# Kernel optimization log

Hardware: AMD Instinct MI355X
Metric: run time of the kernel (lower is better)

## Reference

```python
import jax, jax.numpy as jnp
import numpy as np

IN_DIM = 784   # 28*28
N_FEAT = 100
MW = 20
MP = 100
S = 30
N = 2048
BETA = 0.9
THRESH = 1.0


def setup_inputs() -> dict:
    key = jax.random.key(0)
    ks = jax.random.split(key, 6)
    X = jax.random.uniform(ks[0], (N, IN_DIM), jnp.float32)
    r1 = (1.0 / IN_DIM) ** 0.5
    W1 = jax.random.uniform(ks[1], (IN_DIM, N_FEAT), jnp.float32, -r1, r1)
    B1 = jax.random.uniform(ks[2], (N_FEAT,), jnp.float32, -r1, r1)
    r2 = (1.0 / N_FEAT) ** 0.5
    # all mw windows concatenated: (n_feat, mw*mp)
    W2 = jax.random.uniform(ks[3], (N_FEAT, MW * MP), jnp.float32, -r2, r2)
    B2 = jax.random.uniform(ks[4], (MW * MP,), jnp.float32, -r2, r2)
    # uniform noise for Bernoulli rate coding (spikegen.rate)
    U = jax.random.uniform(ks[5], (S, N, N_FEAT), jnp.float32)
    return {"X": X, "W1": W1, "B1": B1, "W2": W2, "B2": B2, "U": U}


def reference(X, W1, B1, W2, B2, U):
    # Feature layer: linear -> sigmoid(./3) -> Bernoulli rate-coded spikes
    Z_prob = jax.nn.sigmoid((X @ W1 + B1) / 3.0)          # (N, F)
    Z_spk = (U < Z_prob[None]).astype(X.dtype)             # (S, N, F) in {0,1}

    # Enhancement: one GEMM per run covering all windows (LIF is elementwise,
    # so concatenating the mw window weight matrices is exact).
    H_pre = jnp.einsum('snf,fp->snp', Z_spk, W2) + B2      # (S, N, MW*MP)

    # LIF (snn.Leaky, reset-by-subtraction):
    #   mem_t = beta*mem_{t-1} + x_t - spk_{t-1}*thresh ; spk_t = (mem_t > thresh)
    def step(carry, x):
        mem, spk = carry
        mem = BETA * mem + x - spk * THRESH
        spk = (mem > THRESH).astype(x.dtype)
        return (mem, spk), spk

    z0 = jnp.zeros(H_pre.shape[1:], H_pre.dtype)
    _, H_spk = jax.lax.scan(step, (z0, z0), H_pre)         # (S, N, MW*MP)

    # Rate aggregation over time, then concat [Z | H]
    A = jnp.concatenate([Z_spk.mean(axis=0), H_spk.mean(axis=0)], axis=1)
    return A  # (N, N_FEAT + MW*MP)
```

## Files before the change

kernel.cpp:

```cpp
#include <hip/hip_runtime.h>

#define NN      2048
#define IN_DIM  784
#define NFEAT   100
#define NP      2000
#define NS      30
#define OUTC    2100
#define NWIN    5
#define G2      2
#define GB      4
#define CHUNK   64

typedef double f64x4  __attribute__((ext_vector_type(4)));
typedef float  f32x4  __attribute__((ext_vector_type(4)));
typedef short  bf16x8 __attribute__((ext_vector_type(8)));

#define AS1 __attribute__((address_space(1)))
#define AS3 __attribute__((address_space(3)))

__device__ __forceinline__ void stage16(const void* g, void* l) {
    __builtin_amdgcn_global_load_lds((const AS1 unsigned int*)g,
                                     (AS3 unsigned int*)l, 16, 0, 0);
}

__device__ __forceinline__ f64x4 mfma_f64(double a, double b, f64x4 c) {
#if __has_builtin(__builtin_amdgcn_mfma_f64_16x16x4f64)
    return __builtin_amdgcn_mfma_f64_16x16x4f64(a, b, c, 0, 0, 0);
#else
    asm volatile("v_mfma_f64_16x16x4_f64 %0, %1, %2, %0"
                 : "+v"(c) : "v"(a), "v"(b));
    return c;
#endif
}

__global__ __launch_bounds__(128) void sbls_k1(
    const float* __restrict__ X, const float* __restrict__ W1,
    const float* __restrict__ B1, const float* __restrict__ U,
    float* __restrict__ out, unsigned* __restrict__ colmask)
{
    __shared__ float xs[IN_DIM];
    const int n = blockIdx.x;
    const int t = threadIdx.x;

    for (int k = t; k < IN_DIM; k += 128)
        xs[k] = X[(size_t)n * IN_DIM + k];
    __syncthreads();

    if (t >= NFEAT) return;
    const int f = t;

    double a0 = 0.0, a1 = 0.0, a2 = 0.0, a3 = 0.0;
    for (int k = 0; k < IN_DIM; k += 4) {
        a0 += (double)xs[k + 0] * (double)W1[(k + 0) * NFEAT + f];
        a1 += (double)xs[k + 1] * (double)W1[(k + 1) * NFEAT + f];
        a2 += (double)xs[k + 2] * (double)W1[(k + 2) * NFEAT + f];
        a3 += (double)xs[k + 3] * (double)W1[(k + 3) * NFEAT + f];
    }
    double acc = (double)B1[f] + ((a0 + a1) + (a2 + a3));
    double z = 1.0 / (1.0 + exp(-acc / 3.0));

    unsigned m = 0;
    int cnt = 0;
    for (int s = 0; s < NS; ++s) {
        float u = U[(size_t)s * (NN * NFEAT) + (size_t)n * NFEAT + f];
        int sp = ((double)u < z) ? 1 : 0;
        m |= (unsigned)sp << s;
        cnt += sp;
    }
    colmask[n * NFEAT + f] = m;
    out[(size_t)n * OUTC + f] = (float)((double)cnt / 30.0);
}

__global__ __launch_bounds__(256) void sbls_slice(
    const float* __restrict__ W2, unsigned short* __restrict__ slt)
{
    int idx = blockIdx.x * blockDim.x + threadIdx.x;
    if (idx >= NP * 128) return;
    int f = idx & 127;
    int p = idx >> 7;

    double w = (f < NFEAT) ? (double)W2[(size_t)f * NP + p] : 0.0;
    double aw = fabs(w);
    double sg = (w < 0.0) ? -1.0 : 1.0;
    double r = aw;
    const double scale[NWIN] = {0x1p11, 0x1p19, 0x1p27, 0x1p35, 0x1p43};
#pragma unroll
    for (int j = 0; j < NWIN; ++j) {
        double t = floor(r * scale[j]);
        r = r - t / scale[j];
        float v = (float)(sg * t / scale[j]);
        unsigned u = __builtin_bit_cast(unsigned, v);
        slt[((size_t)j * NP + p) * 128 + f] = (unsigned short)(u >> 16);
    }
}

__global__ __launch_bounds__(256) void sbls_afrag2(
    const unsigned* __restrict__ colmask, unsigned short* __restrict__ afragG)
{
    __shared__ unsigned smask[G2][NFEAT];
    const int ng = blockIdx.x;
    const int t  = threadIdx.x;

    for (int i = t; i < G2 * NFEAT; i += 256)
        smask[i / NFEAT][i % NFEAT] = colmask[ng * G2 * NFEAT + i];
    __syncthreads();

    for (int e = t; e < 16 * 64; e += 256) {
        int fid = e >> 6, L = e & 63;
        int st = fid & 1, n = (fid >> 1) & 1, kt = fid >> 2;
        int lgE = L >> 4, lmE = L & 15;
        int s = st * 16 + lmE;
        bf16x8 v;
#pragma unroll
        for (int j = 0; j < 8; ++j) {
            int f = kt * 32 + lgE * 8 + j;
            unsigned mv = (f < NFEAT) ? smask[n][f] : 0u;
            v[j] = (short)(((mv >> s) & 1u) ? 0x3F80 : 0);
        }
        *(bf16x8*)(afragG + ((size_t)ng * 16 + fid) * 64 * 8 + (size_t)L * 8) = v;
    }
}

union ShA {
    unsigned short b[2][NWIN][64][32];
    double h[G2][32][67];
};

__global__ __launch_bounds__(256, 4) void sbls_k2_ga(
    const unsigned short* __restrict__ slt,
    const unsigned short* __restrict__ afragG,
    const float*    __restrict__ B2,
    float*          __restrict__ out)
{
    __shared__ __align__(16) ShA sh;

    const int ng    = blockIdx.x;
    const int chunk = blockIdx.y;
    const int t  = threadIdx.x;
    const int l  = t & 63;
    const int wv = t >> 6;
    const int lm = l & 15;
    const int lg = l >> 4;

    const int plw = wv * 16 + (l >> 2);
    const int pw  = chunk * CHUNK + plw;
    const int prw = (pw < NP) ? pw : (NP - 1);
    const int fgw = ((l & 3) - ((l >> 3) & 3)) & 3;
    const unsigned short* sbase = slt + (size_t)prw * 128 + fgw * 8;

    const unsigned short* ag = afragG + (size_t)ng * 16 * 64 * 8;

    const int prd = wv * 16 + lm;
    const int slot0 = (lm >> 1) & 3;

#define STAGE(buf, kt)                                                        \
    {                                                                         \
        _Pragma("unroll")                                                     \
        for (int w = 0; w < NWIN; ++w)                                        \
            stage16(sbase + (size_t)w * NP * 128 + (kt) * 32,                 \
                    &sh.b[buf][w][wv * 16][0]);                               \
    }

    f32x4 acc[3][2][G2];
#pragma unroll
    for (int wp = 0; wp < 3; ++wp)
#pragma unroll
        for (int st = 0; st < 2; ++st)
#pragma unroll
            for (int n = 0; n < G2; ++n)
                acc[wp][st][n] = (f32x4){0.f, 0.f, 0.f, 0.f};

    STAGE(0, 0)
    bf16x8 acur[G2][2], anxt[G2][2];
#pragma unroll
    for (int n = 0; n < G2; ++n)
#pragma unroll
        for (int st = 0; st < 2; ++st)
            acur[n][st] = *(const bf16x8*)(
                ag + ((size_t)((0 * G2 + n) * 2 + st) * 64 + l) * 8);
    __syncthreads();

#pragma unroll
    for (int kt = 0; kt < 4; ++kt) {
        const int buf = kt & 1;
        if (kt < 3) {
            STAGE(buf ^ 1, kt + 1)
#pragma unroll
            for (int n = 0; n < G2; ++n)
#pragma unroll
                for (int st = 0; st < 2; ++st)
                    anxt[n][st] = *(const bf16x8*)(
                        ag + ((size_t)(((kt + 1) * G2 + n) * 2 + st) * 64 + l) * 8);
        }

        bf16x8 b[NWIN];
#pragma unroll
        for (int w = 0; w < NWIN; ++w) {
            const int slot = (lg + slot0) & 3;
            b[w] = *(const bf16x8*)(&sh.b[buf][w][prd][slot * 8]);
        }

#pragma unroll
        for (int w = 0; w < NWIN; ++w)
#pragma unroll
            for (int n = 0; n < G2; ++n)
#pragma unroll
                for (int st = 0; st < 2; ++st)
                    acc[w >> 1][st][n] = __builtin_amdgcn_mfma_f32_16x16x32_bf16(
                        acur[n][st], b[w], acc[w >> 1][st][n], 0, 0, 0);

        __syncthreads();
        if (kt < 3) {
#pragma unroll
            for (int n = 0; n < G2; ++n)
#pragma unroll
                for (int st = 0; st < 2; ++st)
                    acur[n][st] = anxt[n][st];
        }
    }
#undef STAGE

#pragma unroll
    for (int n = 0; n < G2; ++n)
#pragma unroll
        for (int st = 0; st < 2; ++st)
#pragma unroll
            for (int r = 0; r < 4; ++r) {
                double hv = (double)acc[0][st][n][r]
                          + (double)acc[1][st][n][r]
                          + (double)acc[2][st][n][r];
                sh.h[n][st * 16 + lg * 4 + r][wv * 16 + lm] = hv;
            }
    __syncthreads();
    if (t < 64 * G2) {
        const int nn = t >> 6;
        const int pl = t & 63;
        const int pp = chunk * CHUNK + pl;
        if (pp < NP) {
            double b2d = (double)B2[pp];
            double mem = 0.0, spk = 0.0;
            int cnt = 0;
#pragma unroll
            for (int s = 0; s < NS; ++s) {
                double hh = sh.h[nn][s][pl] + b2d;
                mem = 0.9 * mem + hh - spk;
                bool sp = mem > 1.0;
                spk = sp ? 1.0 : 0.0;
                cnt += sp;
            }
            out[(size_t)(ng * G2 + nn) * OUTC + NFEAT + pp] = (float)((double)cnt / 30.0);
        }
    }
}

__global__ __launch_bounds__(256, 2) void sbls_k2_bf16(
    const unsigned short* __restrict__ slt,
    const float*    __restrict__ B2,
    const unsigned* __restrict__ colmask,
    float*          __restrict__ out)
{
    __shared__ unsigned smask[GB][NFEAT];
    union ShU {
        unsigned short afrag[32][64][8];
        double h[GB][32][67];
    };
    __shared__ __align__(16) ShU shu;

    const int ng    = blockIdx.x;
    const int chunk = blockIdx.y;
    const int t  = threadIdx.x;
    const int l  = t & 63;
    const int wv = t >> 6;
    const int lm = l & 15;
    const int lg = l >> 4;

    for (int i = t; i < GB * NFEAT; i += 256)
        smask[i / NFEAT][i % NFEAT] = colmask[(ng * GB + i / NFEAT) * NFEAT + (i % NFEAT)];
    __syncthreads();

    for (int e = t; e < 32 * 64; e += 256) {
        int fid = e >> 6, L = e & 63;
        int st = fid & 1, n = (fid >> 1) & 3, kt = fid >> 3;
        int lgE = L >> 4, lmE = L & 15;
        int s = st * 16 + lmE;
        bf16x8 v;
#pragma unroll
        for (int j = 0; j < 8; ++j) {
            int f = kt * 32 + lgE * 8 + j;
            unsigned mv = (f < NFEAT) ? smask[n][f] : 0u;
            v[j] = (short)(((mv >> s) & 1u) ? 0x3F80 : 0);
        }
        *(bf16x8*)(&shu.afrag[fid][L][0]) = v;
    }
    __syncthreads();

    const int p = chunk * CHUNK + wv * 16 + lm;
    const int prow = (p < NP) ? p : (NP - 1);
    const unsigned short* bbase = slt + (size_t)prow * 128 + lg * 8;

    f32x4 acc[3][2][GB];
#pragma unroll
    for (int wp = 0; wp < 3; ++wp)
#pragma unroll
        for (int st = 0; st < 2; ++st)
#pragma unroll
            for (int n = 0; n < GB; ++n)
                acc[wp][st][n] = (f32x4){0.f, 0.f, 0.f, 0.f};

    bf16x8 bcur[NWIN], bnxt[NWIN];
#pragma unroll
    for (int w = 0; w < NWIN; ++w)
        bcur[w] = *(const bf16x8*)(bbase + (size_t)w * NP * 128);

#pragma unroll
    for (int kt = 0; kt < 4; ++kt) {
        bf16x8 a[GB][2];
#pragma unroll
        for (int n = 0; n < GB; ++n)
#pragma unroll
            for (int st = 0; st < 2; ++st)
                a[n][st] = *(const bf16x8*)(&shu.afrag[(kt * GB + n) * 2 + st][l][0]);

        if (kt < 3) {
#pragma unroll
            for (int w = 0; w < NWIN; ++w)
                bnxt[w] = *(const bf16x8*)(bbase + (size_t)w * NP * 128 + (kt + 1) * 32);
        }

#pragma unroll
        for (int w = 0; w < NWIN; ++w)
#pragma unroll
            for (int n = 0; n < GB; ++n)
#pragma unroll
                for (int st = 0; st < 2; ++st)
                    acc[w >> 1][st][n] = __builtin_amdgcn_mfma_f32_16x16x32_bf16(
                        a[n][st], bcur[w], acc[w >> 1][st][n], 0, 0, 0);

        if (kt < 3) {
#pragma unroll
            for (int w = 0; w < NWIN; ++w) bcur[w] = bnxt[w];
        }
    }

    __syncthreads();
#pragma unroll
    for (int n = 0; n < GB; ++n)
#pragma unroll
        for (int st = 0; st < 2; ++st)
#pragma unroll
            for (int r = 0; r < 4; ++r) {
                double hv = (double)acc[0][st][n][r]
                          + (double)acc[1][st][n][r]
                          + (double)acc[2][st][n][r];
                shu.h[n][st * 16 + lg * 4 + r][wv * 16 + lm] = hv;
            }
    __syncthreads();
    {
        const int nn = t >> 6;
        const int pl = t & 63;
        const int pp = chunk * CHUNK + pl;
        if (pp < NP) {
            double b2d = (double)B2[pp];
            double mem = 0.0, spk = 0.0;
            int cnt = 0;
#pragma unroll
            for (int s = 0; s < NS; ++s) {
                double hh = shu.h[nn][s][pl] + b2d;
                mem = 0.9 * mem + hh - spk;
                bool sp = mem > 1.0;
                spk = sp ? 1.0 : 0.0;
                cnt += sp;
            }
            out[(size_t)(ng * GB + nn) * OUTC + NFEAT + pp] = (float)((double)cnt / 30.0);
        }
    }
}

__global__ __launch_bounds__(256, 2) void sbls_k2_f64(
    const float*    __restrict__ W2, const float* __restrict__ B2,
    const unsigned* __restrict__ colmask, float* __restrict__ out)
{
    __shared__ unsigned smask[NFEAT];
    __shared__ double h_lds[32][130];

    const int n     = blockIdx.x;
    const int chunk = blockIdx.y;
    const int l  = threadIdx.x & 63;
    const int wv = threadIdx.x >> 6;
    const int lm = l & 15;
    const int lg = l >> 4;

    if (threadIdx.x < NFEAT)
        smask[threadIdx.x] = colmask[n * NFEAT + threadIdx.x];

    f64x4 zero = (f64x4){0.0, 0.0, 0.0, 0.0};
    f64x4 d1 = mfma_f64((double)lm, 1.0, zero);
    f64x4 d2 = mfma_f64(1.0, (double)lm, zero);
    int srow[4], pcol[4];
#pragma unroll
    for (int r = 0; r < 4; ++r) {
        int a = (int)(d1[r] * 0.25);
        int b = (int)(d2[r] * 0.25);
        srow[r] = (a < 0) ? 0 : (a > 15 ? 15 : a);
        pcol[r] = (b < 0) ? 0 : (b > 15 ? 15 : b);
    }
    __syncthreads();

    f64x4 acc[2][4];
    int pclamp[4];
#pragma unroll
    for (int i = 0; i < 4; ++i) {
        int p = chunk * 256 + (wv * 4 + i) * 16 + lm;
        pclamp[i] = (p < NP) ? p : (NP - 1);
        acc[0][i] = zero; acc[1][i] = zero;
    }
    for (int kt = 0; kt < 25; ++kt) {
        unsigned mw = smask[kt * 4 + lg];
        double a0 = ((mw >> lm) & 1u) ? 1.0 : 0.0;
        double a1 = ((mw >> (lm + 16)) & 1u) ? 1.0 : 0.0;
        const float* wrow = W2 + (size_t)(kt * 4 + lg) * NP;
#pragma unroll
        for (int i = 0; i < 4; ++i) {
            double b = (double)wrow[pclamp[i]];
            acc[0][i] = mfma_f64(a0, b, acc[0][i]);
            acc[1][i] = mfma_f64(a1, b, acc[1][i]);
        }
    }
#pragma unroll
    for (int hp = 0; hp < 2; ++hp) {
        __syncthreads();
        if ((wv >> 1) == hp) {
#pragma unroll
            for (int i = 0; i < 4; ++i) {
                int tloc = (wv & 1) * 4 + i;
#pragma unroll
                for (int st = 0; st < 2; ++st)
#pragma unroll
                    for (int r = 0; r < 4; ++r)
                        h_lds[st * 16 + srow[r]][tloc * 16 + pcol[r]] = acc[st][i][r];
            }
        }
        __syncthreads();
        if (threadIdx.x < 128) {
            int p = chunk * 256 + hp * 128 + threadIdx.x;
            if (p < NP) {
                double b2d = (double)B2[p];
                double mem = 0.0, spk = 0.0;
                int cnt = 0;
#pragma unroll
                for (int s = 0; s < NS; ++s) {
                    double hh = h_lds[s][threadIdx.x] + b2d;
                    mem = 0.9 * mem + hh - spk;
                    bool sp = mem > 1.0;
                    spk = sp ? 1.0 : 0.0;
                    cnt += sp;
                }
                out[(size_t)n * OUTC + NFEAT + p] = (float)((double)cnt / 30.0);
            }
        }
    }
}

extern "C" void kernel_launch(void* const* d_in, const int* in_sizes, int n_in,
                              void* d_out, int out_size, void* d_ws, size_t ws_size,
                              hipStream_t stream) {
    const float* X  = (const float*)d_in[0];
    const float* W1 = (const float*)d_in[1];
    const float* B1 = (const float*)d_in[2];
    const float* W2 = (const float*)d_in[3];
    const float* B2 = (const float*)d_in[4];
    const float* U  = (const float*)d_in[5];
    float* out = (float*)d_out;

    unsigned* colmask = (unsigned*)d_ws;
    const size_t SLT_OFF   = 1u << 20;
    const size_t SLT_BYTES = (size_t)NWIN * NP * 128 * 2;
    const size_t AF_OFF    = 4u << 20;
    const size_t AF_BYTES  = (size_t)(NN / G2) * 16 * 64 * 8 * 2;
    unsigned short* slt    = (unsigned short*)((char*)d_ws + SLT_OFF);
    unsigned short* afragG = (unsigned short*)((char*)d_ws + AF_OFF);
    bool tierA = (ws_size >= AF_OFF + AF_BYTES);
    bool tierB = (ws_size >= SLT_OFF + SLT_BYTES);

    sbls_k1<<<NN, 128, 0, stream>>>(X, W1, B1, U, out, colmask);

    if (tierA) {
        sbls_slice<<<(NP * 128 + 255) / 256, 256, 0, stream>>>(W2, slt);
        sbls_afrag2<<<NN / G2, 256, 0, stream>>>(colmask, afragG);
        dim3 grid(NN / G2, (NP + CHUNK - 1) / CHUNK);
        sbls_k2_ga<<<grid, 256, 0, stream>>>(slt, afragG, B2, out);
    } else if (tierB) {
        sbls_slice<<<(NP * 128 + 255) / 256, 256, 0, stream>>>(W2, slt);
        dim3 grid(NN / GB, (NP + CHUNK - 1) / CHUNK);
        sbls_k2_bf16<<<grid, 256, 0, stream>>>(slt, B2, colmask, out);
    } else {
        dim3 grid(NN, (NP + 255) / 256);
        sbls_k2_f64<<<grid, 256, 0, stream>>>(W2, B2, colmask, out);
    }
}
```

Baseline: 236.9 us.

## Process four samples per block with XCD-aware block remapping and MFMA priority

Doubles the number of samples per block in the main spike-GEMM kernel, from two to four, so each staged W2 slice tile in LDS is reused across more MFMAs. Blocks are remapped so that consecutive sample groups are placed on the same XCD, which aims to improve L2 locality for the A fragments. The A-fragment prefetch double buffer is replaced by a load issued after the MFMAs, and s_setprio is raised around the MFMA burst. In exchange the kernel uses more accumulator registers (occupancy hint lowered from 4 to 3), and the LIF epilogue now runs in two sequential passes through shared memory.

```diff
diff --git a/kernel.cpp b/kernel.cpp
--- a/kernel.cpp
+++ b/kernel.cpp
@@ -7,7 +7,7 @@
 #define NS      30
 #define OUTC    2100
 #define NWIN    5
-#define G2      2
+#define G4      4
 #define GB      4
 #define CHUNK   64
 
@@ -94,20 +94,20 @@
     }
 }
 
-__global__ __launch_bounds__(256) void sbls_afrag2(
+__global__ __launch_bounds__(256) void sbls_afrag4(
     const unsigned* __restrict__ colmask, unsigned short* __restrict__ afragG)
 {
-    __shared__ unsigned smask[G2][NFEAT];
+    __shared__ unsigned smask[G4][NFEAT];
     const int ng = blockIdx.x;
     const int t  = threadIdx.x;
 
-    for (int i = t; i < G2 * NFEAT; i += 256)
-        smask[i / NFEAT][i % NFEAT] = colmask[ng * G2 * NFEAT + i];
-    __syncthreads();
-
-    for (int e = t; e < 16 * 64; e += 256) {
+    for (int i = t; i < G4 * NFEAT; i += 256)
+        smask[i / NFEAT][i % NFEAT] = colmask[ng * G4 * NFEAT + i];
+    __syncthreads();
+
+    for (int e = t; e < 32 * 64; e += 256) {
         int fid = e >> 6, L = e & 63;
-        int st = fid & 1, n = (fid >> 1) & 1, kt = fid >> 2;
+        int st = fid & 1, n = (fid >> 1) & 3, kt = fid >> 3;
         int lgE = L >> 4, lmE = L & 15;
         int s = st * 16 + lmE;
         bf16x8 v;
@@ -117,16 +117,16 @@
             unsigned mv = (f < NFEAT) ? smask[n][f] : 0u;
             v[j] = (short)(((mv >> s) & 1u) ? 0x3F80 : 0);
         }
-        *(bf16x8*)(afragG + ((size_t)ng * 16 + fid) * 64 * 8 + (size_t)L * 8) = v;
+        *(bf16x8*)(afragG + ((size_t)ng * 32 + fid) * 64 * 8 + (size_t)L * 8) = v;
     }
 }
 
 union ShA {
     unsigned short b[2][NWIN][64][32];
-    double h[G2][32][67];
+    double h[2][32][67];
 };
 
-__global__ __launch_bounds__(256, 4) void sbls_k2_ga(
+__global__ __launch_bounds__(256, 3) void sbls_k2_ga(
     const unsigned short* __restrict__ slt,
     const unsigned short* __restrict__ afragG,
     const float*    __restrict__ B2,
@@ -134,8 +134,12 @@
 {
     __shared__ __align__(16) ShA sh;
 
-    const int ng    = blockIdx.x;
-    const int chunk = blockIdx.y;
+    const int lid  = blockIdx.y * 512 + blockIdx.x;
+    const int xcd  = lid & 7;
+    const int idx  = lid >> 3;
+    const int chunk = idx & 31;
+    const int ng    = xcd * 64 + (idx >> 5);
+
     const int t  = threadIdx.x;
     const int l  = t & 63;
     const int wv = t >> 6;
@@ -148,7 +152,7 @@
     const int fgw = ((l & 3) - ((l >> 3) & 3)) & 3;
     const unsigned short* sbase = slt + (size_t)prw * 128 + fgw * 8;
 
-    const unsigned short* ag = afragG + (size_t)ng * 16 * 64 * 8;
+    const unsigned short* ag = afragG + (size_t)ng * 32 * 64 * 8;
 
     const int prd = wv * 16 + lm;
     const int slot0 = (lm >> 1) & 3;
@@ -161,37 +165,29 @@
                     &sh.b[buf][w][wv * 16][0]);                               \
     }
 
-    f32x4 acc[3][2][G2];
+    f32x4 acc[3][2][G4];
 #pragma unroll
     for (int wp = 0; wp < 3; ++wp)
 #pragma unroll
         for (int st = 0; st < 2; ++st)
 #pragma unroll
-            for (int n = 0; n < G2; ++n)
+            for (int n = 0; n < G4; ++n)
                 acc[wp][st][n] = (f32x4){0.f, 0.f, 0.f, 0.f};
 
     STAGE(0, 0)
-    bf16x8 acur[G2][2], anxt[G2][2];
-#pragma unroll
-    for (int n = 0; n < G2; ++n)
+    bf16x8 acur[G4][2];
+#pragma unroll
+    for (int n = 0; n < G4; ++n)
 #pragma unroll
         for (int st = 0; st < 2; ++st)
             acur[n][st] = *(const bf16x8*)(
-                ag + ((size_t)((0 * G2 + n) * 2 + st) * 64 + l) * 8);
+                ag + ((size_t)((0 * G4 + n) * 2 + st) * 64 + l) * 8);
     __syncthreads();
 
 #pragma unroll
     for (int kt = 0; kt < 4; ++kt) {
         const int buf = kt & 1;
-        if (kt < 3) {
-            STAGE(buf ^ 1, kt + 1)
-#pragma unroll
-            for (int n = 0; n < G2; ++n)
-#pragma unroll
-                for (int st = 0; st < 2; ++st)
-                    anxt[n][st] = *(const bf16x8*)(
-                        ag + ((size_t)(((kt + 1) * G2 + n) * 2 + st) * 64 + l) * 8);
-        }
+        if (kt < 3) STAGE(buf ^ 1, kt + 1)
 
         bf16x8 b[NWIN];
 #pragma unroll
@@ -200,56 +196,66 @@
             b[w] = *(const bf16x8*)(&sh.b[buf][w][prd][slot * 8]);
         }
 
+        __builtin_amdgcn_s_setprio(1);
 #pragma unroll
         for (int w = 0; w < NWIN; ++w)
 #pragma unroll
-            for (int n = 0; n < G2; ++n)
+            for (int n = 0; n < G4; ++n)
 #pragma unroll
                 for (int st = 0; st < 2; ++st)
                     acc[w >> 1][st][n] = __builtin_amdgcn_mfma_f32_16x16x32_bf16(
                         acur[n][st], b[w], acc[w >> 1][st][n], 0, 0, 0);
-
+        __builtin_amdgcn_s_setprio(0);
+
+        if (kt < 3) {
+#pragma unroll
+            for (int n = 0; n < G4; ++n)
+#pragma unroll
+                for (int st = 0; st < 2; ++st)
+                    acur[n][st] = *(const bf16x8*)(
+                        ag + ((size_t)(((kt + 1) * G4 + n) * 2 + st) * 64 + l) * 8);
+        }
         __syncthreads();
-        if (kt < 3) {
-#pragma unroll
-            for (int n = 0; n < G2; ++n)
-#pragma unroll
-                for (int st = 0; st < 2; ++st)
-                    acur[n][st] = anxt[n][st];
-        }
     }
 #undef STAGE
 
 #pragma unroll
-    for (int n = 0; n < G2; ++n)
-#pragma unroll
-        for (int st = 0; st < 2; ++st)
-#pragma unroll
-            for (int r = 0; r < 4; ++r) {
-                double hv = (double)acc[0][st][n][r]
-                          + (double)acc[1][st][n][r]
-                          + (double)acc[2][st][n][r];
-                sh.h[n][st * 16 + lg * 4 + r][wv * 16 + lm] = hv;
+    for (int np2 = 0; np2 < 2; ++np2) {
+#pragma unroll
+        for (int nn = 0; nn < 2; ++nn) {
+            const int n = np2 * 2 + nn;
+#pragma unroll
+            for (int st = 0; st < 2; ++st)
+#pragma unroll
+                for (int r = 0; r < 4; ++r) {
+                    double hv = (double)acc[0][st][n][r]
+                              + (double)acc[1][st][n][r]
+                              + (double)acc[2][st][n][r];
+                    sh.h[nn][st * 16 + lg * 4 + r][wv * 16 + lm] = hv;
+                }
+        }
+        __syncthreads();
+        if (t < 128) {
+            const int nn = t >> 6;
+            const int pl = t & 63;
+            const int pp = chunk * CHUNK + pl;
+            if (pp < NP) {
+                double b2d = (double)B2[pp];
+                double mem = 0.0, spk = 0.0;
+                int cnt = 0;
+#pragma unroll
+                for (int s = 0; s < NS; ++s) {
+                    double hh = sh.h[nn][s][pl] + b2d;
+                    mem = 0.9 * mem + hh - spk;
+                    bool sp = mem > 1.0;
+                    spk = sp ? 1.0 : 0.0;
+                    cnt += sp;
+                }
+                out[(size_t)(ng * G4 + np2 * 2 + nn) * OUTC + NFEAT + pp] =
+                    (float)((double)cnt / 30.0);
             }
-    __syncthreads();
-    if (t < 64 * G2) {
-        const int nn = t >> 6;
-        const int pl = t & 63;
-        const int pp = chunk * CHUNK + pl;
-        if (pp < NP) {
-            double b2d = (double)B2[pp];
-            double mem = 0.0, spk = 0.0;
-            int cnt = 0;
-#pragma unroll
-            for (int s = 0; s < NS; ++s) {
-                double hh = sh.h[nn][s][pl] + b2d;
-                mem = 0.9 * mem + hh - spk;
-                bool sp = mem > 1.0;
-                spk = sp ? 1.0 : 0.0;
-                cnt += sp;
-            }
-            out[(size_t)(ng * G2 + nn) * OUTC + NFEAT + pp] = (float)((double)cnt / 30.0);
-        }
+        }
+        if (np2 == 0) __syncthreads();
     }
 }
 
@@ -476,7 +482,7 @@
     const size_t SLT_OFF   = 1u << 20;
     const size_t SLT_BYTES = (size_t)NWIN * NP * 128 * 2;
     const size_t AF_OFF    = 4u << 20;
-    const size_t AF_BYTES  = (size_t)(NN / G2) * 16 * 64 * 8 * 2;
+    const size_t AF_BYTES  = (size_t)(NN / G4) * 32 * 64 * 8 * 2;
     unsigned short* slt    = (unsigned short*)((char*)d_ws + SLT_OFF);
     unsigned short* afragG = (unsigned short*)((char*)d_ws + AF_OFF);
     bool tierA = (ws_size >= AF_OFF + AF_BYTES);
@@ -486,8 +492,8 @@
 
     if (tierA) {
         sbls_slice<<<(NP * 128 + 255) / 256, 256, 0, stream>>>(W2, slt);
-        sbls_afrag2<<<NN / G2, 256, 0, stream>>>(colmask, afragG);
-        dim3 grid(NN / G2, (NP + CHUNK - 1) / CHUNK);
+        sbls_afrag4<<<NN / G4, 256, 0, stream>>>(colmask, afragG);
+        dim3 grid(512, 32);
         sbls_k2_ga<<<grid, 256, 0, stream>>>(slt, afragG, B2, out);
     } else if (tierB) {
         sbls_slice<<<(NP * 128 + 255) / 256, 256, 0, stream>>>(W2, slt);
```

Result: faster. 215.3 us (-9.1%).
